# Optimization experiments

Measured on AMD Instinct MI355X. Metric: run time of the kernel, lower is better.

## Reference

```python
import jax, jax.numpy as jnp
import numpy as np

E = 8            # num_experts
D_IN = 2         # in_features (xy coords)
D_OUT = 3        # out_features (rgb)
H = 256          # hidden_features
N_HIDDEN = 3     # num_layers=4 -> 1 first sine layer + 3 hidden sine layers + final linear
OMEGA = 30.0
N = 65536        # number of coordinate points (256x256)


def setup_inputs() -> dict:
    key = jax.random.key(0)
    ks = jax.random.split(key, 10)
    x = jax.random.uniform(ks[0], (N, D_IN), dtype=jnp.float32) * 2.0 - 1.0
    # gate: Linear(D_IN, E)
    gate_W = jax.random.normal(ks[1], (D_IN, E), dtype=jnp.float32) / np.sqrt(D_IN)
    gate_b = jnp.zeros((E,), dtype=jnp.float32)
    # SIREN init: first layer U(-1/in, 1/in), hidden U(-sqrt(6/in)/omega, sqrt(6/in)/omega)
    W0 = jax.random.uniform(ks[2], (E, D_IN, H), dtype=jnp.float32,
                            minval=-1.0 / D_IN, maxval=1.0 / D_IN)
    b0 = jax.random.uniform(ks[3], (E, H), dtype=jnp.float32,
                            minval=-1.0 / np.sqrt(D_IN), maxval=1.0 / np.sqrt(D_IN))
    wlim = np.sqrt(6.0 / H) / OMEGA
    Wh = jax.random.uniform(ks[4], (E, N_HIDDEN, H, H), dtype=jnp.float32,
                            minval=-wlim, maxval=wlim)
    bh = jax.random.uniform(ks[5], (E, N_HIDDEN, H), dtype=jnp.float32,
                            minval=-1.0 / np.sqrt(H), maxval=1.0 / np.sqrt(H))
    Wout = jax.random.uniform(ks[6], (E, H, D_OUT), dtype=jnp.float32,
                              minval=-1.0 / np.sqrt(H), maxval=1.0 / np.sqrt(H))
    bout = jax.random.uniform(ks[7], (E, D_OUT), dtype=jnp.float32,
                              minval=-1.0 / np.sqrt(H), maxval=1.0 / np.sqrt(H))
    return {"x": x, "gate_W": gate_W, "gate_b": gate_b,
            "W0": W0, "b0": b0, "Wh": Wh, "bh": bh,
            "Wout": Wout, "bout": bout}


def reference(x, gate_W, gate_b, W0, b0, Wh, bh, Wout, bout):
    # gate: softmax(Linear(x))  -> [N, E]
    gates = jax.nn.softmax(x @ gate_W + gate_b, axis=-1)
    # all experts evaluated densely via batched GEMMs over expert axis e
    h = jnp.sin(OMEGA * (jnp.einsum('ni,eih->enh', x, W0) + b0[:, None, :]))  # [E,N,H]
    for l in range(N_HIDDEN):
        h = jnp.sin(OMEGA * (jnp.einsum('enh,eho->eno', h, Wh[:, l]) + bh[:, l][:, None, :]))
    expert_out = jnp.einsum('enh,eho->eno', h, Wout) + bout[:, None, :]      # [E,N,D_OUT]
    # softmax-gated weighted sum over experts -> [N, D_OUT]
    combined = jnp.einsum('ne,eno->no', gates, expert_out)
    return combined
```

## Files before the change

### kernel.cpp

```cpp
#include <hip/hip_runtime.h>
#include <math.h>

#define E_ 8
#define H_ 256
#define N_ 65536
#define NHID_ 3
#define MT 64
#define HPAD 264
#define OMEGA_ 30.0f
#define REV_SCALE 4.7746482927568605f

#define PWH_ELEMS (E_ * NHID_ * 8 * 16 * 64 * 8)
#define PWO_ELEMS (E_ * 8 * 64 * 8)
#define WS_NEEDED (2 * (size_t)PWH_ELEMS * 2 + 2 * (size_t)PWO_ELEMS * 2)

typedef __attribute__((ext_vector_type(8))) __bf16 bf16x8;
typedef __attribute__((ext_vector_type(4))) float f32x4;

__device__ __forceinline__ void split_bf16(float v, __bf16& hi, __bf16& lo) {
  hi = (__bf16)v;
  lo = (__bf16)(v - (float)hi);
}

__device__ __forceinline__ void sin_store(float z_rev, __bf16* h_hi, int idx) {
  const float s = __builtin_amdgcn_sinf(__builtin_amdgcn_fractf(z_rev));
  h_hi[idx] = (__bf16)s;
}

__global__ void zero_out_k(float* __restrict__ out) {
  out[blockIdx.x * 256 + threadIdx.x] = 0.0f;
}

__global__ void pack_wh_k(const float* __restrict__ Wh,
                          __bf16* __restrict__ Phi, __bf16* __restrict__ Plo) {
  int t = blockIdx.x * 256 + threadIdx.x;
  int lane = t & 63;
  int r = t >> 6;
  int nb = r & 15;
  int kb = (r >> 4) & 7;
  int el = r >> 7;
  int n  = nb * 16 + (lane & 15);
  int k0 = kb * 32 + (lane >> 4) * 8;
  const float* src = Wh + (size_t)el * (H_ * H_);
  __bf16* dhi = Phi + (size_t)t * 8;
  __bf16* dlo = Plo + (size_t)t * 8;
#pragma unroll
  for (int j = 0; j < 8; ++j) {
    __bf16 hi, lo;
    split_bf16(src[(size_t)(k0 + j) * H_ + n] * REV_SCALE, hi, lo);
    dhi[j] = hi; dlo[j] = lo;
  }
}

__global__ void pack_wout_k(const float* __restrict__ Wout,
                            __bf16* __restrict__ Phi, __bf16* __restrict__ Plo) {
  int t = blockIdx.x * 256 + threadIdx.x;
  int lane = t & 63;
  int kb = (t >> 6) & 7;
  int e  = t >> 9;
  int n  = lane & 15;
  int k0 = kb * 32 + (lane >> 4) * 8;
  __bf16* dhi = Phi + (size_t)t * 8;
  __bf16* dlo = Plo + (size_t)t * 8;
#pragma unroll
  for (int j = 0; j < 8; ++j) {
    float v = (n < 3) ? Wout[((size_t)e * H_ + (k0 + j)) * 3 + n] : 0.0f;
    __bf16 hi, lo;
    split_bf16(v, hi, lo);
    dhi[j] = hi; dlo[j] = lo;
  }
}

__global__ __launch_bounds__(256, 4) void moe_main_packed_k(
    const float* __restrict__ x,
    const float* __restrict__ gate_W,
    const float* __restrict__ gate_b,
    const float* __restrict__ W0,
    const float* __restrict__ b0,
    const __bf16* __restrict__ Pwh_hi,
    const __bf16* __restrict__ Pwh_lo,
    const float* __restrict__ bh,
    const __bf16* __restrict__ Pwo_hi,
    const __bf16* __restrict__ Pwo_lo,
    const float* __restrict__ bout,
    float* __restrict__ out)
{
  __shared__ alignas(16) __bf16 h_hi[MT * HPAD];
  __shared__ float gate_s[MT];

  const int e    = blockIdx.y;
  const int m0   = blockIdx.x * MT;
  const int tid  = threadIdx.x;
  const int wave = tid >> 6;
  const int lane = tid & 63;
  const int l15  = lane & 15;
  const int quad = lane >> 4;

  if (tid < MT) {
    const int mg = m0 + tid;
    const float x0 = x[mg * 2 + 0];
    const float x1 = x[mg * 2 + 1];
    float lg[E_];
    float mx = -1e30f;
#pragma unroll
    for (int k = 0; k < E_; ++k) {
      lg[k] = x0 * gate_W[k] + x1 * gate_W[E_ + k] + gate_b[k];
      mx = fmaxf(mx, lg[k]);
    }
    float s = 0.0f;
#pragma unroll
    for (int k = 0; k < E_; ++k) s += __expf(lg[k] - mx);
    gate_s[tid] = __expf(lg[e] - mx) / s;
  }

  {
    const float w0a = W0[(e * 2 + 0) * H_ + tid] * REV_SCALE;
    const float w1a = W0[(e * 2 + 1) * H_ + tid] * REV_SCALE;
    const float bb  = b0[e * H_ + tid] * REV_SCALE;
    for (int m = 0; m < MT; ++m) {
      const float x0 = x[(m0 + m) * 2 + 0];
      const float x1 = x[(m0 + m) * 2 + 1];
      const float z_rev = fmaf(x1, w1a, fmaf(x0, w0a, bb));
      sin_store(z_rev, h_hi, m * HPAD + tid);
    }
  }
  __syncthreads();

  const int nb0 = wave * 4;
  const size_t fragoff = (size_t)(nb0 * 64 + lane) * 8;

#pragma unroll 1
  for (int l = 0; l < NHID_; ++l) {
    const size_t lbase = (size_t)(e * NHID_ + l) * (8 * 16 * 64 * 8);
    const __bf16* pBh = Pwh_hi + lbase + fragoff;
    const float* bhrow = bh + (size_t)(e * NHID_ + l) * H_;

    float bias_rev[4];
#pragma unroll
    for (int nbi = 0; nbi < 4; ++nbi)
      bias_rev[nbi] = bhrow[(nb0 + nbi) * 16 + l15] * REV_SCALE;

    f32x4 acc[4][4];
#pragma unroll
    for (int mt = 0; mt < 4; ++mt)
#pragma unroll
      for (int nbi = 0; nbi < 4; ++nbi)
        acc[mt][nbi] = (f32x4){bias_rev[nbi], bias_rev[nbi], bias_rev[nbi], bias_rev[nbi]};

#pragma unroll 1
    for (int kb = 0; kb < 8; ++kb) {
      bf16x8 bhf[4];
#pragma unroll
      for (int nbi = 0; nbi < 4; ++nbi)
        bhf[nbi] = *reinterpret_cast<const bf16x8*>(pBh + nbi * 512);
      pBh += 16 * 64 * 8;
      const int k0 = kb * 32 + quad * 8;
      bf16x8 ah[4];
#pragma unroll
      for (int mt = 0; mt < 4; ++mt)
        ah[mt] = *reinterpret_cast<const bf16x8*>(&h_hi[(mt * 16 + l15) * HPAD + k0]);
#pragma unroll
      for (int mt = 0; mt < 4; ++mt)
#pragma unroll
        for (int nbi = 0; nbi < 4; ++nbi)
          acc[mt][nbi] = __builtin_amdgcn_mfma_f32_16x16x32_bf16(
              ah[mt], bhf[nbi], acc[mt][nbi], 0, 0, 0);
    }
    __syncthreads();

#pragma unroll
    for (int nbi = 0; nbi < 4; ++nbi) {
      const int n = (nb0 + nbi) * 16 + l15;
#pragma unroll
      for (int mt = 0; mt < 4; ++mt) {
        const int rbase = mt * 16 + quad * 4;
#pragma unroll
        for (int i = 0; i < 4; ++i)
          sin_store(acc[mt][nbi][i], h_hi, (rbase + i) * HPAD + n);
      }
    }
    __syncthreads();
  }

  {
    const __bf16* pOh = Pwo_hi + (size_t)e * (8 * 64 * 8) + (size_t)lane * 8;
    const __bf16* pOl = Pwo_lo + (size_t)e * (8 * 64 * 8) + (size_t)lane * 8;
    f32x4 acco = (f32x4){0.f, 0.f, 0.f, 0.f};
    const int arow = wave * 16 + l15;
#pragma unroll 1
    for (int kb = 0; kb < 8; ++kb) {
      bf16x8 bhf = *reinterpret_cast<const bf16x8*>(pOh);
      bf16x8 blf = *reinterpret_cast<const bf16x8*>(pOl);
      pOh += 512; pOl += 512;
      const int k0 = kb * 32 + quad * 8;
      bf16x8 ah = *reinterpret_cast<const bf16x8*>(&h_hi[arow * HPAD + k0]);
      acco = __builtin_amdgcn_mfma_f32_16x16x32_bf16(ah, blf, acco, 0, 0, 0);
      acco = __builtin_amdgcn_mfma_f32_16x16x32_bf16(ah, bhf, acco, 0, 0, 0);
    }
    if (l15 < 3) {
      const float bo = bout[e * 3 + l15];
      const int rb = wave * 16 + quad * 4;
#pragma unroll
      for (int i = 0; i < 4; ++i) {
        const int m = rb + i;
        const float val = gate_s[m] * (acco[i] + bo);
        atomicAdd(&out[(size_t)(m0 + m) * 3 + l15], val);
      }
    }
  }
}

__global__ __launch_bounds__(256) void moe_main_direct_k(
    const float* __restrict__ x,
    const float* __restrict__ gate_W,
    const float* __restrict__ gate_b,
    const float* __restrict__ W0,
    const float* __restrict__ b0,
    const float* __restrict__ Wh,
    const float* __restrict__ bh,
    const float* __restrict__ Wout,
    const float* __restrict__ bout,
    float* __restrict__ out)
{
  __shared__ alignas(16) __bf16 h_hi[MT * HPAD];
  __shared__ alignas(16) __bf16 h_lo[MT * HPAD];
  __shared__ float gate_s[MT];

  const int e    = blockIdx.y;
  const int m0   = blockIdx.x * MT;
  const int tid  = threadIdx.x;
  const int wave = tid >> 6;
  const int lane = tid & 63;
  const int l15  = lane & 15;
  const int quad = lane >> 4;

  if (tid < MT) {
    const int mg = m0 + tid;
    const float x0 = x[mg * 2 + 0];
    const float x1 = x[mg * 2 + 1];
    float lg[E_];
    float mx = -1e30f;
#pragma unroll
    for (int k = 0; k < E_; ++k) {
      lg[k] = x0 * gate_W[k] + x1 * gate_W[E_ + k] + gate_b[k];
      mx = fmaxf(mx, lg[k]);
    }
    float s = 0.0f;
#pragma unroll
    for (int k = 0; k < E_; ++k) s += __expf(lg[k] - mx);
    gate_s[tid] = __expf(lg[e] - mx) / s;
  }
  {
    const float w0a = W0[(e * 2 + 0) * H_ + tid];
    const float w1a = W0[(e * 2 + 1) * H_ + tid];
    const float bb  = b0[e * H_ + tid];
    for (int m = 0; m < MT; ++m) {
      const float x0 = x[(m0 + m) * 2 + 0];
      const float x1 = x[(m0 + m) * 2 + 1];
      const float z = OMEGA_ * fmaf(x1, w1a, fmaf(x0, w0a, bb));
      const float h = __sinf(z);
      __bf16 hi, lo; split_bf16(h, hi, lo);
      h_hi[m * HPAD + tid] = hi;
      h_lo[m * HPAD + tid] = lo;
    }
  }
  __syncthreads();

  const int nb0 = wave * 4;
#pragma unroll 1
  for (int l = 0; l < NHID_; ++l) {
    const float* WB = Wh + (size_t)(e * NHID_ + l) * (H_ * H_);
    f32x4 acc[4][4];
#pragma unroll
    for (int mt = 0; mt < 4; ++mt)
#pragma unroll
      for (int nbi = 0; nbi < 4; ++nbi)
        acc[mt][nbi] = (f32x4){0.f, 0.f, 0.f, 0.f};

#pragma unroll 2
    for (int kb = 0; kb < 8; ++kb) {
      const int k0 = kb * 32 + quad * 8;
      float bfv[4][8];
#pragma unroll
      for (int nbi = 0; nbi < 4; ++nbi) {
        const float* p = WB + (size_t)k0 * H_ + (nb0 + nbi) * 16 + l15;
#pragma unroll
        for (int j = 0; j < 8; ++j) bfv[nbi][j] = p[(size_t)j * H_];
      }
      bf16x8 ah[4], al[4];
#pragma unroll
      for (int mt = 0; mt < 4; ++mt) {
        ah[mt] = *reinterpret_cast<const bf16x8*>(&h_hi[(mt * 16 + l15) * HPAD + k0]);
        al[mt] = *reinterpret_cast<const bf16x8*>(&h_lo[(mt * 16 + l15) * HPAD + k0]);
      }
      bf16x8 bhf[4], blf[4];
#pragma unroll
      for (int nbi = 0; nbi < 4; ++nbi)
#pragma unroll
        for (int j = 0; j < 8; ++j) {
          __bf16 hi, lo; split_bf16(bfv[nbi][j], hi, lo);
          bhf[nbi][j] = hi; blf[nbi][j] = lo;
        }
#pragma unroll
      for (int mt = 0; mt < 4; ++mt)
#pragma unroll
        for (int nbi = 0; nbi < 4; ++nbi) {
          f32x4 a = acc[mt][nbi];
          a = __builtin_amdgcn_mfma_f32_16x16x32_bf16(al[mt], bhf[nbi], a, 0, 0, 0);
          a = __builtin_amdgcn_mfma_f32_16x16x32_bf16(ah[mt], blf[nbi], a, 0, 0, 0);
          a = __builtin_amdgcn_mfma_f32_16x16x32_bf16(ah[mt], bhf[nbi], a, 0, 0, 0);
          acc[mt][nbi] = a;
        }
    }
    __syncthreads();

    const float* bhrow = bh + (size_t)(e * NHID_ + l) * H_;
#pragma unroll
    for (int nbi = 0; nbi < 4; ++nbi) {
      const int n = (nb0 + nbi) * 16 + l15;
      const float bias = bhrow[n];
#pragma unroll
      for (int mt = 0; mt < 4; ++mt) {
        const int rbase = mt * 16 + quad * 4;
#pragma unroll
        for (int i = 0; i < 4; ++i) {
          const float z = OMEGA_ * (acc[mt][nbi][i] + bias);
          const float h = __sinf(z);
          __bf16 hi, lo; split_bf16(h, hi, lo);
          h_hi[(rbase + i) * HPAD + n] = hi;
          h_lo[(rbase + i) * HPAD + n] = lo;
        }
      }
    }
    __syncthreads();
  }

  {
    const float* WO = Wout + (size_t)e * (H_ * 3);
    f32x4 acco = (f32x4){0.f, 0.f, 0.f, 0.f};
    const int arow = wave * 16 + l15;
#pragma unroll
    for (int kb = 0; kb < 8; ++kb) {
      const int k0 = kb * 32 + quad * 8;
      float bfv[8];
#pragma unroll
      for (int j = 0; j < 8; ++j)
        bfv[j] = (l15 < 3) ? WO[(size_t)(k0 + j) * 3 + l15] : 0.0f;
      bf16x8 ah = *reinterpret_cast<const bf16x8*>(&h_hi[arow * HPAD + k0]);
      bf16x8 al = *reinterpret_cast<const bf16x8*>(&h_lo[arow * HPAD + k0]);
      bf16x8 bhf, blf;
#pragma unroll
      for (int j = 0; j < 8; ++j) {
        __bf16 hi, lo; split_bf16(bfv[j], hi, lo);
        bhf[j] = hi; blf[j] = lo;
      }
      acco = __builtin_amdgcn_mfma_f32_16x16x32_bf16(al, bhf, acco, 0, 0, 0);
      acco = __builtin_amdgcn_mfma_f32_16x16x32_bf16(ah, blf, acco, 0, 0, 0);
      acco = __builtin_amdgcn_mfma_f32_16x16x32_bf16(ah, bhf, acco, 0, 0, 0);
    }
    if (l15 < 3) {
      const float bo = bout[e * 3 + l15];
      const int rb = wave * 16 + quad * 4;
#pragma unroll
      for (int i = 0; i < 4; ++i) {
        const int m = rb + i;
        const float val = gate_s[m] * (acco[i] + bo);
        atomicAdd(&out[(size_t)(m0 + m) * 3 + l15], val);
      }
    }
  }
}

extern "C" void kernel_launch(void* const* d_in, const int* in_sizes, int n_in,
                              void* d_out, int out_size, void* d_ws, size_t ws_size,
                              hipStream_t stream) {
  const float* x     = (const float*)d_in[0];
  const float* gateW = (const float*)d_in[1];
  const float* gateb = (const float*)d_in[2];
  const float* W0    = (const float*)d_in[3];
  const float* b0    = (const float*)d_in[4];
  const float* Wh    = (const float*)d_in[5];
  const float* bh    = (const float*)d_in[6];
  const float* Wout  = (const float*)d_in[7];
  const float* bout  = (const float*)d_in[8];
  float* out = (float*)d_out;

  hipLaunchKernelGGL(zero_out_k, dim3(N_ * 3 / 256), dim3(256), 0, stream, out);

  if (ws_size >= WS_NEEDED) {
    __bf16* Pwh_hi = (__bf16*)d_ws;
    __bf16* Pwh_lo = (__bf16*)((char*)d_ws + (size_t)PWH_ELEMS * 2);
    __bf16* Pwo_hi = (__bf16*)((char*)d_ws + 2 * (size_t)PWH_ELEMS * 2);
    __bf16* Pwo_lo = (__bf16*)((char*)d_ws + 2 * (size_t)PWH_ELEMS * 2 + (size_t)PWO_ELEMS * 2);
    hipLaunchKernelGGL(pack_wh_k,  dim3(768), dim3(256), 0, stream, Wh, Pwh_hi, Pwh_lo);
    hipLaunchKernelGGL(pack_wout_k, dim3(16), dim3(256), 0, stream, Wout, Pwo_hi, Pwo_lo);
    hipLaunchKernelGGL(moe_main_packed_k, dim3(N_ / MT, E_), dim3(256), 0, stream,
                       x, gateW, gateb, W0, b0, Pwh_hi, Pwh_lo, bh, Pwo_hi, Pwo_lo, bout, out);
  } else {
    hipLaunchKernelGGL(moe_main_direct_k, dim3(N_ / MT, E_), dim3(256), 0, stream,
                       x, gateW, gateb, W0, b0, Wh, bh, Wout, bout, out);
  }
}
```

Baseline: 293.9 us.

## Ping-pong two row tiles per block to overlap sine epilogue with MFMA

Each block now processes two 64-row tiles with two LDS buffers. The sine epilogue of one tile's layer is interleaved into the MFMA K-loop of the other tile, and the first-layer sine of the second tile is likewise interleaved. This hides the transcendental and LDS-store work behind matrix instructions and removes a barrier per layer. In exchange it doubles the accumulator registers and LDS per block, so launch bounds drop to 2 blocks per CU and the grid is halved.

```diff
diff --git a/kernel.cpp b/kernel.cpp
--- a/kernel.cpp
+++ b/kernel.cpp
@@ -22,9 +22,9 @@
   lo = (__bf16)(v - (float)hi);
 }
 
-__device__ __forceinline__ void sin_store(float z_rev, __bf16* h_hi, int idx) {
+__device__ __forceinline__ void sin_store(float z_rev, __bf16* h, int idx) {
   const float s = __builtin_amdgcn_sinf(__builtin_amdgcn_fractf(z_rev));
-  h_hi[idx] = (__bf16)s;
+  h[idx] = (__bf16)s;
 }
 
 __global__ void zero_out_k(float* __restrict__ out) {
@@ -71,7 +71,95 @@
   }
 }
 
-__global__ __launch_bounds__(256, 4) void moe_main_packed_k(
+__device__ __forceinline__ void init_acc_bias(f32x4 (&acc)[4][4],
+                                              const float* __restrict__ bhrow,
+                                              int nb0, int l15) {
+  float br[4];
+#pragma unroll
+  for (int nbi = 0; nbi < 4; ++nbi)
+    br[nbi] = bhrow[(nb0 + nbi) * 16 + l15] * REV_SCALE;
+#pragma unroll
+  for (int mt = 0; mt < 4; ++mt)
+#pragma unroll
+    for (int nbi = 0; nbi < 4; ++nbi)
+      acc[mt][nbi] = (f32x4){br[nbi], br[nbi], br[nbi], br[nbi]};
+}
+
+template<int MODE>
+__device__ __forceinline__ void fused_K_seg(
+    const __bf16* __restrict__ pBh,
+    const __bf16* __restrict__ hK,
+    f32x4 (&accK)[4][4],
+    f32x4 (&accE)[4][4],
+    __bf16* __restrict__ hE,
+    const float* __restrict__ x, int m0E,
+    float w0, float w1, float bb,
+    int tid, int l15, int quad, int nb0)
+{
+#pragma unroll
+  for (int c = 0; c < 8; ++c) {
+    bf16x8 bhf[4];
+#pragma unroll
+    for (int nbi = 0; nbi < 4; ++nbi)
+      bhf[nbi] = *reinterpret_cast<const bf16x8*>(pBh + c * 8192 + nbi * 512);
+    const int k0 = c * 32 + quad * 8;
+    bf16x8 ah[4];
+#pragma unroll
+    for (int mt = 0; mt < 4; ++mt)
+      ah[mt] = *reinterpret_cast<const bf16x8*>(&hK[(mt * 16 + l15) * HPAD + k0]);
+#pragma unroll
+    for (int mt = 0; mt < 4; ++mt)
+#pragma unroll
+      for (int nbi = 0; nbi < 4; ++nbi)
+        accK[mt][nbi] = __builtin_amdgcn_mfma_f32_16x16x32_bf16(
+            ah[mt], bhf[nbi], accK[mt][nbi], 0, 0, 0);
+    if (MODE == 0) {
+#pragma unroll
+      for (int j = 0; j < 8; ++j) {
+        const int mt  = c >> 1;
+        const int nbi = (c & 1) * 2 + (j >> 2);
+        const int i   = j & 3;
+        sin_store(accE[mt][nbi][i], hE,
+                  (mt * 16 + quad * 4 + i) * HPAD + (nb0 + nbi) * 16 + l15);
+      }
+    } else {
+#pragma unroll
+      for (int j = 0; j < 8; ++j) {
+        const int r = c * 8 + j;
+        const float xx0 = x[(m0E + r) * 2 + 0];
+        const float xx1 = x[(m0E + r) * 2 + 1];
+        sin_store(fmaf(xx1, w1, fmaf(xx0, w0, bb)), hE, r * HPAD + tid);
+      }
+    }
+  }
+}
+
+__device__ __forceinline__ void fused_out_seg(
+    const __bf16* __restrict__ pOh, const __bf16* __restrict__ pOl,
+    const __bf16* __restrict__ hK, f32x4& accO,
+    f32x4 (&accE)[4][4], __bf16* __restrict__ hE,
+    int wave, int l15, int quad, int nb0)
+{
+  const int arow = wave * 16 + l15;
+#pragma unroll
+  for (int c = 0; c < 8; ++c) {
+    bf16x8 bhf = *reinterpret_cast<const bf16x8*>(pOh + c * 512);
+    bf16x8 blf = *reinterpret_cast<const bf16x8*>(pOl + c * 512);
+    bf16x8 ah  = *reinterpret_cast<const bf16x8*>(&hK[arow * HPAD + c * 32 + quad * 8]);
+    accO = __builtin_amdgcn_mfma_f32_16x16x32_bf16(ah, blf, accO, 0, 0, 0);
+    accO = __builtin_amdgcn_mfma_f32_16x16x32_bf16(ah, bhf, accO, 0, 0, 0);
+#pragma unroll
+    for (int j = 0; j < 8; ++j) {
+      const int mt  = c >> 1;
+      const int nbi = (c & 1) * 2 + (j >> 2);
+      const int i   = j & 3;
+      sin_store(accE[mt][nbi][i], hE,
+                (mt * 16 + quad * 4 + i) * HPAD + (nb0 + nbi) * 16 + l15);
+    }
+  }
+}
+
+__global__ __launch_bounds__(256, 2) void moe_main_packed_k(
     const float* __restrict__ x,
     const float* __restrict__ gate_W,
     const float* __restrict__ gate_b,
@@ -85,18 +173,20 @@
     const float* __restrict__ bout,
     float* __restrict__ out)
 {
-  __shared__ alignas(16) __bf16 h_hi[MT * HPAD];
-  __shared__ float gate_s[MT];
+  __shared__ alignas(16) __bf16 hA[MT * HPAD];
+  __shared__ alignas(16) __bf16 hB[MT * HPAD];
+  __shared__ float gate_s[2 * MT];
 
   const int e    = blockIdx.y;
-  const int m0   = blockIdx.x * MT;
+  const int m0   = blockIdx.x * (2 * MT);
   const int tid  = threadIdx.x;
   const int wave = tid >> 6;
   const int lane = tid & 63;
   const int l15  = lane & 15;
   const int quad = lane >> 4;
-
-  if (tid < MT) {
+  const int nb0  = wave * 4;
+
+  if (tid < 2 * MT) {
     const int mg = m0 + tid;
     const float x0 = x[mg * 2 + 0];
     const float x1 = x[mg * 2 + 1];
@@ -113,98 +203,84 @@
     gate_s[tid] = __expf(lg[e] - mx) / s;
   }
 
+  const float w0a = W0[(e * 2 + 0) * H_ + tid] * REV_SCALE;
+  const float w1a = W0[(e * 2 + 1) * H_ + tid] * REV_SCALE;
+  const float bba = b0[e * H_ + tid] * REV_SCALE;
+
+  for (int m = 0; m < MT; ++m) {
+    const float x0 = x[(m0 + m) * 2 + 0];
+    const float x1 = x[(m0 + m) * 2 + 1];
+    sin_store(fmaf(x1, w1a, fmaf(x0, w0a, bba)), hA, m * HPAD + tid);
+  }
+  __syncthreads();
+
+  const size_t fragoff = (size_t)(nb0 * 64 + lane) * 8;
+  const float* bh_e = bh + (size_t)(e * NHID_) * H_;
+  const __bf16* PB0 = Pwh_hi + (size_t)(e * NHID_ + 0) * (8 * 16 * 64 * 8) + fragoff;
+  const __bf16* PB1 = Pwh_hi + (size_t)(e * NHID_ + 1) * (8 * 16 * 64 * 8) + fragoff;
+  const __bf16* PB2 = Pwh_hi + (size_t)(e * NHID_ + 2) * (8 * 16 * 64 * 8) + fragoff;
+
+  f32x4 accA[4][4], accB[4][4];
+
+  init_acc_bias(accA, bh_e + 0 * H_, nb0, l15);
+  fused_K_seg<1>(PB0, hA, accA, accA, hB, x, m0 + MT, w0a, w1a, bba, tid, l15, quad, nb0);
+  __syncthreads();
+
+  init_acc_bias(accB, bh_e + 0 * H_, nb0, l15);
+  fused_K_seg<0>(PB0, hB, accB, accA, hA, x, 0, 0.f, 0.f, 0.f, tid, l15, quad, nb0);
+  __syncthreads();
+
+  init_acc_bias(accA, bh_e + 1 * H_, nb0, l15);
+  fused_K_seg<0>(PB1, hA, accA, accB, hB, x, 0, 0.f, 0.f, 0.f, tid, l15, quad, nb0);
+  __syncthreads();
+
+  init_acc_bias(accB, bh_e + 1 * H_, nb0, l15);
+  fused_K_seg<0>(PB1, hB, accB, accA, hA, x, 0, 0.f, 0.f, 0.f, tid, l15, quad, nb0);
+  __syncthreads();
+
+  init_acc_bias(accA, bh_e + 2 * H_, nb0, l15);
+  fused_K_seg<0>(PB2, hA, accA, accB, hB, x, 0, 0.f, 0.f, 0.f, tid, l15, quad, nb0);
+  __syncthreads();
+
+  init_acc_bias(accB, bh_e + 2 * H_, nb0, l15);
+  fused_K_seg<0>(PB2, hB, accB, accA, hA, x, 0, 0.f, 0.f, 0.f, tid, l15, quad, nb0);
+  __syncthreads();
+
+  const __bf16* pOh = Pwo_hi + (size_t)e * (8 * 64 * 8) + (size_t)lane * 8;
+  const __bf16* pOl = Pwo_lo + (size_t)e * (8 * 64 * 8) + (size_t)lane * 8;
   {
-    const float w0a = W0[(e * 2 + 0) * H_ + tid] * REV_SCALE;
-    const float w1a = W0[(e * 2 + 1) * H_ + tid] * REV_SCALE;
-    const float bb  = b0[e * H_ + tid] * REV_SCALE;
-    for (int m = 0; m < MT; ++m) {
-      const float x0 = x[(m0 + m) * 2 + 0];
-      const float x1 = x[(m0 + m) * 2 + 1];
-      const float z_rev = fmaf(x1, w1a, fmaf(x0, w0a, bb));
-      sin_store(z_rev, h_hi, m * HPAD + tid);
-    }
-  }
-  __syncthreads();
-
-  const int nb0 = wave * 4;
-  const size_t fragoff = (size_t)(nb0 * 64 + lane) * 8;
-
-#pragma unroll 1
-  for (int l = 0; l < NHID_; ++l) {
-    const size_t lbase = (size_t)(e * NHID_ + l) * (8 * 16 * 64 * 8);
-    const __bf16* pBh = Pwh_hi + lbase + fragoff;
-    const float* bhrow = bh + (size_t)(e * NHID_ + l) * H_;
-
-    float bias_rev[4];
-#pragma unroll
-    for (int nbi = 0; nbi < 4; ++nbi)
-      bias_rev[nbi] = bhrow[(nb0 + nbi) * 16 + l15] * REV_SCALE;
-
-    f32x4 acc[4][4];
-#pragma unroll
-    for (int mt = 0; mt < 4; ++mt)
-#pragma unroll
-      for (int nbi = 0; nbi < 4; ++nbi)
-        acc[mt][nbi] = (f32x4){bias_rev[nbi], bias_rev[nbi], bias_rev[nbi], bias_rev[nbi]};
-
-#pragma unroll 1
-    for (int kb = 0; kb < 8; ++kb) {
-      bf16x8 bhf[4];
-#pragma unroll
-      for (int nbi = 0; nbi < 4; ++nbi)
-        bhf[nbi] = *reinterpret_cast<const bf16x8*>(pBh + nbi * 512);
-      pBh += 16 * 64 * 8;
-      const int k0 = kb * 32 + quad * 8;
-      bf16x8 ah[4];
-#pragma unroll
-      for (int mt = 0; mt < 4; ++mt)
-        ah[mt] = *reinterpret_cast<const bf16x8*>(&h_hi[(mt * 16 + l15) * HPAD + k0]);
-#pragma unroll
-      for (int mt = 0; mt < 4; ++mt)
-#pragma unroll
-        for (int nbi = 0; nbi < 4; ++nbi)
-          acc[mt][nbi] = __builtin_amdgcn_mfma_f32_16x16x32_bf16(
-              ah[mt], bhf[nbi], acc[mt][nbi], 0, 0, 0);
-    }
-    __syncthreads();
-
-#pragma unroll
-    for (int nbi = 0; nbi < 4; ++nbi) {
-      const int n = (nb0 + nbi) * 16 + l15;
-#pragma unroll
-      for (int mt = 0; mt < 4; ++mt) {
-        const int rbase = mt * 16 + quad * 4;
-#pragma unroll
-        for (int i = 0; i < 4; ++i)
-          sin_store(acc[mt][nbi][i], h_hi, (rbase + i) * HPAD + n);
-      }
-    }
-    __syncthreads();
-  }
-
-  {
-    const __bf16* pOh = Pwo_hi + (size_t)e * (8 * 64 * 8) + (size_t)lane * 8;
-    const __bf16* pOl = Pwo_lo + (size_t)e * (8 * 64 * 8) + (size_t)lane * 8;
-    f32x4 acco = (f32x4){0.f, 0.f, 0.f, 0.f};
-    const int arow = wave * 16 + l15;
-#pragma unroll 1
-    for (int kb = 0; kb < 8; ++kb) {
-      bf16x8 bhf = *reinterpret_cast<const bf16x8*>(pOh);
-      bf16x8 blf = *reinterpret_cast<const bf16x8*>(pOl);
-      pOh += 512; pOl += 512;
-      const int k0 = kb * 32 + quad * 8;
-      bf16x8 ah = *reinterpret_cast<const bf16x8*>(&h_hi[arow * HPAD + k0]);
-      acco = __builtin_amdgcn_mfma_f32_16x16x32_bf16(ah, blf, acco, 0, 0, 0);
-      acco = __builtin_amdgcn_mfma_f32_16x16x32_bf16(ah, bhf, acco, 0, 0, 0);
-    }
+    f32x4 accO = (f32x4){0.f, 0.f, 0.f, 0.f};
+    fused_out_seg(pOh, pOl, hA, accO, accB, hB, wave, l15, quad, nb0);
     if (l15 < 3) {
       const float bo = bout[e * 3 + l15];
       const int rb = wave * 16 + quad * 4;
 #pragma unroll
       for (int i = 0; i < 4; ++i) {
         const int m = rb + i;
-        const float val = gate_s[m] * (acco[i] + bo);
-        atomicAdd(&out[(size_t)(m0 + m) * 3 + l15], val);
+        atomicAdd(&out[(size_t)(m0 + m) * 3 + l15], gate_s[m] * (accO[i] + bo));
+      }
+    }
+  }
+  __syncthreads();
+
+  {
+    f32x4 accO = (f32x4){0.f, 0.f, 0.f, 0.f};
+    const int arow = wave * 16 + l15;
+#pragma unroll
+    for (int c = 0; c < 8; ++c) {
+      bf16x8 bhf = *reinterpret_cast<const bf16x8*>(pOh + c * 512);
+      bf16x8 blf = *reinterpret_cast<const bf16x8*>(pOl + c * 512);
+      bf16x8 ah  = *reinterpret_cast<const bf16x8*>(&hB[arow * HPAD + c * 32 + quad * 8]);
+      accO = __builtin_amdgcn_mfma_f32_16x16x32_bf16(ah, blf, accO, 0, 0, 0);
+      accO = __builtin_amdgcn_mfma_f32_16x16x32_bf16(ah, bhf, accO, 0, 0, 0);
+    }
+    if (l15 < 3) {
+      const float bo = bout[e * 3 + l15];
+      const int rb = wave * 16 + quad * 4;
+#pragma unroll
+      for (int i = 0; i < 4; ++i) {
+        const int m = rb + i;
+        atomicAdd(&out[(size_t)(m0 + MT + m) * 3 + l15], gate_s[MT + m] * (accO[i] + bo));
       }
     }
   }
@@ -394,7 +470,7 @@
     __bf16* Pwo_lo = (__bf16*)((char*)d_ws + 2 * (size_t)PWH_ELEMS * 2 + (size_t)PWO_ELEMS * 2);
     hipLaunchKernelGGL(pack_wh_k,  dim3(768), dim3(256), 0, stream, Wh, Pwh_hi, Pwh_lo);
     hipLaunchKernelGGL(pack_wout_k, dim3(16), dim3(256), 0, stream, Wout, Pwo_hi, Pwo_lo);
-    hipLaunchKernelGGL(moe_main_packed_k, dim3(N_ / MT, E_), dim3(256), 0, stream,
+    hipLaunchKernelGGL(moe_main_packed_k, dim3(N_ / (2 * MT), E_), dim3(256), 0, stream,
                        x, gateW, gateb, W0, b0, Pwh_hi, Pwh_lo, bh, Pwo_hi, Pwo_lo, bout, out);
   } else {
     hipLaunchKernelGGL(moe_main_direct_k, dim3(N_ / MT, E_), dim3(256), 0, stream,
```

Result: slower. 306.6 us (+4.3%).
